# Kernel tuning notes

Measured on AMD Instinct MI355X. Metric: run time of the kernel, lower is better.

## Reference

```python
import jax, jax.numpy as jnp
import numpy as np

B, S, E, H = 2, 2048, 512, 8
D = E // H  # head_dim = 64


def setup_inputs() -> dict:
    key = jax.random.key(0)
    ks = jax.random.split(key, 10)
    sc = 1.0 / np.sqrt(E)
    x = jax.random.normal(ks[0], (B, S, E), dtype=jnp.float32)
    # parent index per node: tree_structure[b][parent[b,i]] contains i
    parent = jax.random.randint(ks[1], (B, S), 0, S, dtype=jnp.int32)
    Wp = jax.random.normal(ks[2], (E, E), dtype=jnp.float32) * sc
    bp = jnp.zeros((E,), dtype=jnp.float32)
    Wc = jax.random.normal(ks[3], (E, E), dtype=jnp.float32) * sc
    bc = jnp.zeros((E,), dtype=jnp.float32)
    Ws = jax.random.normal(ks[4], (E, E), dtype=jnp.float32) * sc
    bs = jnp.zeros((E,), dtype=jnp.float32)
    Wo = jax.random.normal(ks[5], (E, E), dtype=jnp.float32) * sc
    bo = jnp.zeros((E,), dtype=jnp.float32)
    return {"x": x, "parent": parent, "Wp": Wp, "bp": bp, "Wc": Wc,
            "bc": bc, "Ws": Ws, "bs": bs, "Wo": Wo, "bo": bo}


def _tree_mask(parent):
    # Vectorized equivalent of the per-batch scatter loop:
    # mask[b, p, c] = mask[b, c, p] = 1 for each (parent, child) edge.
    b_idx = jnp.arange(B)[:, None]
    rows = jnp.arange(S)[None, :]
    m = jnp.zeros((B, S, S), dtype=bool)
    m = m.at[b_idx, rows, parent].set(True)
    m = m.at[b_idx, parent, rows].set(True)
    return m  # (B, S, S), broadcast over heads


def reference(x, parent, Wp, bp, Wc, bc, Ws, bs, Wo, bo):
    # Tri-projection
    p = (x @ Wp + bp).reshape(B, S, H, D)
    c = (x @ Wc + bc).reshape(B, S, H, D)
    s = (x @ Ws + bs).reshape(B, S, H, D)
    scores = jnp.einsum('bnhd,bmhd->bnhm', p, c) / jnp.sqrt(jnp.float32(D))
    mask = _tree_mask(parent)  # (B, S, S)
    scores = jnp.where(mask[:, :, None, :], scores, -jnp.inf)
    attn = jax.nn.softmax(scores, axis=-1)  # dropout is identity (train=False)
    out = jnp.einsum('bnhm,bmhd->bnhd', attn, s).reshape(B, S, E)
    return out @ Wo + bo
```

## Files before the change

kernel.cpp:

```cpp
#include <hip/hip_runtime.h>
#include <hip/hip_bf16.h>

#define B_  2
#define S_  2048
#define E_  512
#define H_  8
#define D_  64
#define BS_ (B_ * S_)
#define N1_ 1536
#define K_  512

typedef __bf16 bf16x8 __attribute__((ext_vector_type(8)));
typedef float  f32x4  __attribute__((ext_vector_type(4)));
typedef unsigned short us8 __attribute__((ext_vector_type(8)));

__device__ __forceinline__ ushort f2bf(float f) {
    unsigned u = __float_as_uint(f);
    unsigned r = (u + 0x7FFFu + ((u >> 16) & 1u)) >> 16;
    return (ushort)r;
}
__device__ __forceinline__ float bf2f(ushort b) {
    return __uint_as_float(((unsigned)b) << 16);
}

__device__ __forceinline__ void gld_lds16(const ushort* g, ushort* l) {
    __builtin_amdgcn_global_load_lds(
        (const __attribute__((address_space(1))) unsigned int*)g,
        (__attribute__((address_space(3))) unsigned int*)l, 16, 0, 0);
}

__global__ __launch_bounds__(256) void prep_kernel(
    const float* __restrict__ x, ushort* __restrict__ xb,
    const float* __restrict__ Wp, const float* __restrict__ Wc,
    const float* __restrict__ Ws, const float* __restrict__ Wo,
    ushort* __restrict__ Wcat_t, ushort* __restrict__ Wo_t) {
    int bid = blockIdx.x;
    int tid = threadIdx.x;
    if (bid < 2048) {
        int i = bid * 256 + tid;
        float4 v = ((const float4*)x)[i];
        ushort4 o;
        o.x = f2bf(v.x); o.y = f2bf(v.y); o.z = f2bf(v.z); o.w = f2bf(v.w);
        ((ushort4*)xb)[i] = o;
        return;
    }
    __shared__ ushort T[64][65];
    int bid2 = bid - 2048;
    int z = bid2 >> 6;
    int t = bid2 & 63;
    const float* src = (z == 0) ? Wp : (z == 1) ? Wc : (z == 2) ? Ws : Wo;
    ushort* dst = (z < 3) ? (Wcat_t + (size_t)z * 512 * 512) : Wo_t;
    int n0 = (t & 7) * 64, k0 = (t >> 3) * 64;
    int g = tid >> 6, l = tid & 63;
    #pragma unroll
    for (int r = 0; r < 16; r++) {
        int kk = g * 16 + r;
        T[kk][l] = f2bf(src[(size_t)(k0 + kk) * 512 + n0 + l]);
    }
    __syncthreads();
    #pragma unroll
    for (int r = 0; r < 16; r++) {
        int nn = g * 16 + r;
        dst[(size_t)(n0 + nn) * 512 + k0 + l] = T[l][nn];
    }
}

template<int TM, int TN, bool BF16OUT>
__global__ __launch_bounds__(256) void gemm_mfma_kernel(
    const ushort* __restrict__ A,
    const ushort* __restrict__ Bt,
    const float*  __restrict__ b0,
    const float*  __restrict__ b1,
    const float*  __restrict__ b2,
    void* __restrict__ Cv,
    int N, int K) {
    constexpr int TK = 64;
    constexpr int FM = TM / 32;
    constexpr int NF = TN / 32;
    __shared__ ushort As[TM][TK];
    __shared__ ushort Bs[TN][TK];

    const int tid  = threadIdx.x;
    const int lane = tid & 63;
    const int wave = tid >> 6;
    const int wm = wave >> 1, wn = wave & 1;
    const int row0 = blockIdx.y * TM;
    const int col0 = blockIdx.x * TN;

    f32x4 acc[FM][NF] = {};

    const int srow = lane >> 3;
    const int scol = (lane & 7) * 8;

    const int lrow = lane & 15;
    const int lk   = (lane >> 4) * 8;

    for (int kt = 0; kt < K; kt += TK) {
        const ushort* ga = A + (size_t)(row0 + wave * (TM / 4) + srow) * K + kt + scol;
        #pragma unroll
        for (int j = 0; j < FM; j++)
            gld_lds16(ga + (size_t)j * 8 * K, &As[wave * (TM / 4) + j * 8][0]);
        const ushort* gb = Bt + (size_t)(col0 + wave * (TN / 4) + srow) * K + kt + scol;
        #pragma unroll
        for (int j = 0; j < NF; j++)
            gld_lds16(gb + (size_t)j * 8 * K, &Bs[wave * (TN / 4) + j * 8][0]);
        __syncthreads();

        #pragma unroll
        for (int kk = 0; kk < TK; kk += 32) {
            bf16x8 af[FM], bfr[NF];
            #pragma unroll
            for (int i = 0; i < FM; i++)
                af[i] = *(const bf16x8*)(&As[wm * (FM * 16) + i * 16 + lrow][kk + lk]);
            #pragma unroll
            for (int j = 0; j < NF; j++)
                bfr[j] = *(const bf16x8*)(&Bs[wn * (TN / 2) + j * 16 + lrow][kk + lk]);
            #pragma unroll
            for (int i = 0; i < FM; i++)
                #pragma unroll
                for (int j = 0; j < NF; j++)
                    acc[i][j] = __builtin_amdgcn_mfma_f32_16x16x32_bf16(
                        af[i], bfr[j], acc[i][j], 0, 0, 0);
        }
        __syncthreads();
    }

    const int ccol = lane & 15;
    const int crow = (lane >> 4) * 4;
    #pragma unroll
    for (int j = 0; j < NF; j++) {
        int gcol = col0 + wn * (TN / 2) + j * 16 + ccol;
        float bias = (gcol < 512) ? b0[gcol]
                   : (gcol < 1024) ? b1[gcol - 512] : b2[gcol - 1024];
        #pragma unroll
        for (int i = 0; i < FM; i++) {
            int grow = row0 + wm * (FM * 16) + i * 16 + crow;
            #pragma unroll
            for (int rg = 0; rg < 4; rg++) {
                float v = acc[i][j][rg] + bias;
                if (BF16OUT)
                    ((ushort*)Cv)[(size_t)(grow + rg) * N + gcol] = f2bf(v);
                else
                    ((float*)Cv)[(size_t)(grow + rg) * N + gcol] = v;
            }
        }
    }
}

__global__ __launch_bounds__(256) void attn_gather_kernel(
    const ushort* __restrict__ PCS, const int* __restrict__ parent,
    ushort* __restrict__ attn) {
    int gtid = blockIdx.x * blockDim.x + threadIdx.x;
    int w    = gtid >> 6;
    int lane = gtid & 63;
    int bbase = ((w >> 11) << 11);
    int i  = w & (S_ - 1);
    int rp = bbase + parent[w];

    float pnf[8];
    {
        us8 p8 = *(const us8*)(PCS + (size_t)w * N1_ + lane * 8);
        #pragma unroll
        for (int j = 0; j < 8; j++) pnf[j] = bf2f(p8[j]);
    }

    float Z, av[8];
    {
        const ushort* rm = PCS + (size_t)rp * N1_;
        us8 c8 = *(const us8*)(rm + 512  + lane * 8);
        us8 s8 = *(const us8*)(rm + 1024 + lane * 8);
        float t = 0.f;
        #pragma unroll
        for (int j = 0; j < 8; j++) t += pnf[j] * bf2f(c8[j]);
        t += __shfl_xor(t, 1); t += __shfl_xor(t, 2); t += __shfl_xor(t, 4);
        float e = __expf(t * 0.125f);
        Z = e;
        #pragma unroll
        for (int j = 0; j < 8; j++) av[j] = e * bf2f(s8[j]);
    }

    for (int t0 = 0; t0 < S_; t0 += 256) {
        int4 pv = *(const int4*)(parent + bbase + t0 + lane * 4);
        int pc[4] = {pv.x, pv.y, pv.z, pv.w};
        #pragma unroll
        for (int jj = 0; jj < 4; jj++) {
            unsigned long long mask = __ballot(pc[jj] == i);
            while (mask) {
                int l = __ffsll(mask) - 1;
                mask &= mask - 1;
                int c = bbase + t0 + l * 4 + jj;
                if (c == rp) continue;
                const ushort* rc = PCS + (size_t)c * N1_;
                us8 c8 = *(const us8*)(rc + 512  + lane * 8);
                us8 s8 = *(const us8*)(rc + 1024 + lane * 8);
                float t = 0.f;
                #pragma unroll
                for (int j = 0; j < 8; j++) t += pnf[j] * bf2f(c8[j]);
                t += __shfl_xor(t, 1); t += __shfl_xor(t, 2); t += __shfl_xor(t, 4);
                float e = __expf(t * 0.125f);
                Z += e;
                #pragma unroll
                for (int j = 0; j < 8; j++) av[j] += e * bf2f(s8[j]);
            }
        }
    }

    float rz = 1.0f / Z;
    us8 o8;
    #pragma unroll
    for (int j = 0; j < 8; j++) o8[j] = f2bf(av[j] * rz);
    *(us8*)(attn + (size_t)w * E_ + lane * 8) = o8;
}

extern "C" void kernel_launch(void* const* d_in, const int* in_sizes, int n_in,
                              void* d_out, int out_size, void* d_ws, size_t ws_size,
                              hipStream_t stream) {
    const float* x      = (const float*)d_in[0];
    const int*   parent = (const int*)  d_in[1];
    const float* Wp     = (const float*)d_in[2];
    const float* bp     = (const float*)d_in[3];
    const float* Wc     = (const float*)d_in[4];
    const float* bc     = (const float*)d_in[5];
    const float* Ws     = (const float*)d_in[6];
    const float* bs     = (const float*)d_in[7];
    const float* Wo     = (const float*)d_in[8];
    const float* bo     = (const float*)d_in[9];
    float* out = (float*)d_out;

    char* ws = (char*)d_ws;
    ushort* x_bf    = (ushort*)(ws + 0);
    ushort* Wcat_t  = (ushort*)(ws + 4194304);
    ushort* Wo_t    = (ushort*)(ws + 5767168);
    ushort* PCS_bf  = (ushort*)(ws + 6291456);
    ushort* attn_bf = (ushort*)(ws + 18874368);

    prep_kernel<<<2304, 256, 0, stream>>>(x, x_bf, Wp, Wc, Ws, Wo, Wcat_t, Wo_t);

    gemm_mfma_kernel<128, 96, true>
        <<<dim3(N1_ / 96, BS_ / 128), 256, 0, stream>>>(
        x_bf, Wcat_t, bp, bc, bs, PCS_bf, N1_, K_);

    attn_gather_kernel<<<BS_ * 64 / 256, 256, 0, stream>>>(
        PCS_bf, parent, attn_bf);

    gemm_mfma_kernel<64, 64, false>
        <<<dim3(E_ / 64, BS_ / 64), 256, 0, stream>>>(
        attn_bf, Wo_t, bo, bo, bo, out, E_, K_);
}
```

Measured before the change: 114.0 us.

## Double-buffer LDS tiles in MFMA GEMM and swizzle block order

The GEMM kernel now keeps two LDS buffers and issues the async global-to-LDS loads for the next K tile before computing on the current one, so memory latency overlaps MFMA work. Workgroup indices are also remapped with a stride-8 swizzle to improve cache locality between neighbouring blocks. The cost is double the LDS use, which may lower occupancy, and a swizzle that assumes the workgroup count is a multiple of eight.

```diff
diff --git a/kernel.cpp b/kernel.cpp
--- a/kernel.cpp
+++ b/kernel.cpp
@@ -77,15 +77,20 @@
     constexpr int TK = 64;
     constexpr int FM = TM / 32;
     constexpr int NF = TN / 32;
-    __shared__ ushort As[TM][TK];
-    __shared__ ushort Bs[TN][TK];
+    __shared__ ushort As[2][TM][TK];
+    __shared__ ushort Bs[2][TN][TK];
 
     const int tid  = threadIdx.x;
     const int lane = tid & 63;
     const int wave = tid >> 6;
     const int wm = wave >> 1, wn = wave & 1;
-    const int row0 = blockIdx.y * TM;
-    const int col0 = blockIdx.x * TN;
+
+    const int nbx = gridDim.x;
+    const int nwg = gridDim.x * gridDim.y;
+    const int lin = blockIdx.y * nbx + blockIdx.x;
+    const int swz = (lin & 7) * (nwg >> 3) + (lin >> 3);
+    const int row0 = (swz / nbx) * TM;
+    const int col0 = (swz % nbx) * TN;
 
     f32x4 acc[FM][NF] = {};
 
@@ -95,26 +100,36 @@
     const int lrow = lane & 15;
     const int lk   = (lane >> 4) * 8;
 
-    for (int kt = 0; kt < K; kt += TK) {
-        const ushort* ga = A + (size_t)(row0 + wave * (TM / 4) + srow) * K + kt + scol;
+    const ushort* gab = A  + (size_t)(row0 + wave * (TM / 4) + srow) * K + scol;
+    const ushort* gbb = Bt + (size_t)(col0 + wave * (TN / 4) + srow) * K + scol;
+
+    auto stage = [&](int buf, int kt) {
+        const ushort* ga = gab + kt;
         #pragma unroll
         for (int j = 0; j < FM; j++)
-            gld_lds16(ga + (size_t)j * 8 * K, &As[wave * (TM / 4) + j * 8][0]);
-        const ushort* gb = Bt + (size_t)(col0 + wave * (TN / 4) + srow) * K + kt + scol;
+            gld_lds16(ga + (size_t)j * 8 * K, &As[buf][wave * (TM / 4) + j * 8][0]);
+        const ushort* gb = gbb + kt;
         #pragma unroll
         for (int j = 0; j < NF; j++)
-            gld_lds16(gb + (size_t)j * 8 * K, &Bs[wave * (TN / 4) + j * 8][0]);
-        __syncthreads();
-
+            gld_lds16(gb + (size_t)j * 8 * K, &Bs[buf][wave * (TN / 4) + j * 8][0]);
+    };
+
+    stage(0, 0);
+    __syncthreads();
+
+    const int nt = K / TK;
+    int cur = 0;
+    for (int t = 0; t < nt; t++) {
+        if (t + 1 < nt) stage(cur ^ 1, (t + 1) * TK);
         #pragma unroll
         for (int kk = 0; kk < TK; kk += 32) {
             bf16x8 af[FM], bfr[NF];
             #pragma unroll
             for (int i = 0; i < FM; i++)
-                af[i] = *(const bf16x8*)(&As[wm * (FM * 16) + i * 16 + lrow][kk + lk]);
+                af[i] = *(const bf16x8*)(&As[cur][wm * (FM * 16) + i * 16 + lrow][kk + lk]);
             #pragma unroll
             for (int j = 0; j < NF; j++)
-                bfr[j] = *(const bf16x8*)(&Bs[wn * (TN / 2) + j * 16 + lrow][kk + lk]);
+                bfr[j] = *(const bf16x8*)(&Bs[cur][wn * (TN / 2) + j * 16 + lrow][kk + lk]);
             #pragma unroll
             for (int i = 0; i < FM; i++)
                 #pragma unroll
@@ -123,6 +138,7 @@
                         af[i], bfr[j], acc[i][j], 0, 0, 0);
         }
         __syncthreads();
+        cur ^= 1;
     }
 
     const int ccol = lane & 15;
```

Measured after the change: 116.4 us. 2.1% more time.
